# Optimization experiments

Measured on AMD Instinct MI355X. Metric: run time of the kernel, lower is better.

## Reference

```python
import jax, jax.numpy as jnp
import numpy as np

N_LOW, N_HIGH = 20000, 60000
E_LOW, E_L2H, E_HIGH = 320000, 540000, 480000
EPS = 1e-5
NEG_SLOPE = 0.2


def _gatv2(x_src, x_dst, edge_index, Wl, Wr, att, bias):
    """PyG GATv2Conv with concat heads, aggr='mean', no self loops.
    att: [H, C]. Returns [n_dst, H*C]."""
    H, C = att.shape
    n_dst = x_dst.shape[0]
    xl = (x_src @ Wl).reshape(-1, H, C)   # [n_src, H, C]
    xr = (x_dst @ Wr).reshape(-1, H, C)   # [n_dst, H, C]
    src, dst = edge_index[0], edge_index[1]
    z = jax.nn.leaky_relu(xl[src] + xr[dst], NEG_SLOPE)        # [E, H, C]
    logits = jnp.einsum('ehc,hc->eh', z, att)                  # [E, H]
    m = jax.ops.segment_max(logits, dst, num_segments=n_dst)   # segment softmax
    e = jnp.exp(logits - m[dst])
    s = jax.ops.segment_sum(e, dst, num_segments=n_dst)
    alpha = e / s[dst]                                         # [E, H]
    out = jax.ops.segment_sum(xl[src] * alpha[:, :, None], dst, num_segments=n_dst)
    deg = jax.ops.segment_sum(jnp.ones((src.shape[0],), out.dtype), dst, num_segments=n_dst)
    out = out / jnp.maximum(deg, 1.0)[:, None, None]           # aggr='mean'
    out = out.reshape(n_dst, H * C)
    if bias is not None:
        out = out + bias
    return out


def _bn(x, g, b):
    mu = x.mean(axis=0)
    var = x.var(axis=0)
    return (x - mu) * jax.lax.rsqrt(var + EPS) * g + b


def _forward(x_low, x_high, z_std, e_low, e_l2h, e_high,
             l1_Wl, l1_Wr, l1_att, l1_b, bn1_g, bn1_b,
             l2_Wl, l2_Wr, l2_att, l2_b, bn2_g, bn2_b,
             l3_Wl, l3_Wr, l3_att, l3_b,
             lh_Wl, lh_Wr, lh_att,
             h1_Wl, h1_Wr, h1_att, h1_b, bn3_g, bn3_b,
             h2_Wl, h2_Wr, h2_att, h2_b, bn4_g, bn4_b,
             h3_Wl, h3_Wr, h3_att, h3_b):
    # low_net: GATv2(125->128,h2) -> BN(256) -> GATv2(256->128) -> BN(128) -> GATv2(128->128)
    h = _gatv2(x_low, x_low, e_low, l1_Wl, l1_Wr, l1_att, l1_b)
    h = _bn(h, bn1_g, bn1_b)
    h = _gatv2(h, h, e_low, l2_Wl, l2_Wr, l2_att, l2_b)
    h = _bn(h, bn2_g, bn2_b)
    h = _gatv2(h, h, e_low, l3_Wl, l3_Wr, l3_att, l3_b)
    # bipartite low2high: (encod_low[128], x_high[1]) -> 128, no bias
    eh = _gatv2(h, x_high, e_l2h, lh_Wl, lh_Wr, lh_att, None)
    eh = jnp.concatenate([z_std, eh], axis=-1)                 # [N_HIGH, 129]
    # high_net
    g = _gatv2(eh, eh, e_high, h1_Wl, h1_Wr, h1_att, h1_b)
    g = _bn(g, bn3_g, bn3_b)
    g = _gatv2(g, g, e_high, h2_Wl, h2_Wr, h2_att, h2_b)
    g = _bn(g, bn4_g, bn4_b)
    return _gatv2(g, g, e_high, h3_Wl, h3_Wr, h3_att, h3_b)   # [N_HIGH, 2]


def setup_inputs() -> dict:
    key = jax.random.key(0)
    ks = iter(jax.random.split(key, 64))
    def P(shape, fan_in):
        return jax.random.normal(next(ks), shape, jnp.float32) / np.sqrt(fan_in)
    inp = {}
    inp['x_low'] = jax.random.normal(next(ks), (N_LOW, 125), jnp.float32)
    inp['x_high'] = jax.random.normal(next(ks), (N_HIGH, 1), jnp.float32)
    inp['z_std'] = jax.random.normal(next(ks), (N_HIGH, 1), jnp.float32)
    inp['e_low'] = jnp.stack([jax.random.randint(next(ks), (E_LOW,), 0, N_LOW),
                              jax.random.randint(next(ks), (E_LOW,), 0, N_LOW)])
    inp['e_l2h'] = jnp.stack([jax.random.randint(next(ks), (E_L2H,), 0, N_LOW),
                              jax.random.randint(next(ks), (E_L2H,), 0, N_HIGH)])
    inp['e_high'] = jnp.stack([jax.random.randint(next(ks), (E_HIGH,), 0, N_HIGH),
                               jax.random.randint(next(ks), (E_HIGH,), 0, N_HIGH)])
    inp['l1_Wl'] = P((125, 256), 125); inp['l1_Wr'] = P((125, 256), 125)
    inp['l1_att'] = P((2, 128), 128);  inp['l1_b'] = jnp.zeros((256,), jnp.float32)
    inp['bn1_g'] = jnp.ones((256,), jnp.float32); inp['bn1_b'] = jnp.zeros((256,), jnp.float32)
    inp['l2_Wl'] = P((256, 128), 256); inp['l2_Wr'] = P((256, 128), 256)
    inp['l2_att'] = P((1, 128), 128);  inp['l2_b'] = jnp.zeros((128,), jnp.float32)
    inp['bn2_g'] = jnp.ones((128,), jnp.float32); inp['bn2_b'] = jnp.zeros((128,), jnp.float32)
    inp['l3_Wl'] = P((128, 128), 128); inp['l3_Wr'] = P((128, 128), 128)
    inp['l3_att'] = P((1, 128), 128);  inp['l3_b'] = jnp.zeros((128,), jnp.float32)
    inp['lh_Wl'] = P((128, 128), 128); inp['lh_Wr'] = P((1, 128), 1)
    inp['lh_att'] = P((1, 128), 128)
    inp['h1_Wl'] = P((129, 256), 129); inp['h1_Wr'] = P((129, 256), 129)
    inp['h1_att'] = P((2, 128), 128);  inp['h1_b'] = jnp.zeros((256,), jnp.float32)
    inp['bn3_g'] = jnp.ones((256,), jnp.float32); inp['bn3_b'] = jnp.zeros((256,), jnp.float32)
    inp['h2_Wl'] = P((256, 128), 256); inp['h2_Wr'] = P((256, 128), 256)
    inp['h2_att'] = P((1, 128), 128);  inp['h2_b'] = jnp.zeros((128,), jnp.float32)
    inp['bn4_g'] = jnp.ones((128,), jnp.float32); inp['bn4_b'] = jnp.zeros((128,), jnp.float32)
    inp['h3_Wl'] = P((128, 2), 128);   inp['h3_Wr'] = P((128, 2), 128)
    inp['h3_att'] = P((1, 2), 2);      inp['h3_b'] = jnp.zeros((2,), jnp.float32)
    return inp


def reference(x_low, x_high, z_std, e_low, e_l2h, e_high,
              l1_Wl, l1_Wr, l1_att, l1_b, bn1_g, bn1_b,
              l2_Wl, l2_Wr, l2_att, l2_b, bn2_g, bn2_b,
              l3_Wl, l3_Wr, l3_att, l3_b,
              lh_Wl, lh_Wr, lh_att,
              h1_Wl, h1_Wr, h1_att, h1_b, bn3_g, bn3_b,
              h2_Wl, h2_Wr, h2_att, h2_b, bn4_g, bn4_b,
              h3_Wl, h3_Wr, h3_att, h3_b):
    return _forward(x_low, x_high, z_std, e_low, e_l2h, e_high,
                    l1_Wl, l1_Wr, l1_att, l1_b, bn1_g, bn1_b,
                    l2_Wl, l2_Wr, l2_att, l2_b, bn2_g, bn2_b,
                    l3_Wl, l3_Wr, l3_att, l3_b,
                    lh_Wl, lh_Wr, lh_att,
                    h1_Wl, h1_Wr, h1_att, h1_b, bn3_g, bn3_b,
                    h2_Wl, h2_Wr, h2_att, h2_b, bn4_g, bn4_b,
                    h3_Wl, h3_Wr, h3_att, h3_b)
```

## Files before the change

kernel.cpp:

```cpp
#include <hip/hip_runtime.h>
#include <hip/hip_bf16.h>
#include <cstdint>
#include <cstddef>
#include <cmath>

#define NEG_SLOPE 0.2f

#define PB  1024
#define CSH 10
#define CBS 1024
#define NBCMAX 160
#define PBN 2048

using frag = __attribute__((ext_vector_type(8))) short;
using facc = __attribute__((ext_vector_type(4))) float;

__device__ __forceinline__ float bf_hi(unsigned u) {
    union { unsigned i; float f; } t; t.i = u & 0xffff0000u; return t.f;
}
__device__ __forceinline__ float bf_lo(unsigned u) {
    union { unsigned i; float f; } t; t.i = u << 16; return t.f;
}
__device__ __forceinline__ void unpack8(uint4 u, float* v) {
    v[0] = bf_lo(u.x); v[1] = bf_hi(u.x);
    v[2] = bf_lo(u.y); v[3] = bf_hi(u.y);
    v[4] = bf_lo(u.z); v[5] = bf_hi(u.z);
    v[6] = bf_lo(u.w); v[7] = bf_hi(u.w);
}

typedef const __attribute__((address_space(1))) void* gas_cptr;
typedef __attribute__((address_space(3))) void* las_ptr;
__device__ __forceinline__ void gload_lds16(const __hip_bfloat16* g, __hip_bfloat16* l) {
    __builtin_amdgcn_global_load_lds((gas_cptr)(const void*)g, (las_ptr)(void*)l, 16, 0, 0);
}

__global__ __launch_bounds__(256)
void msplitA(const int* __restrict__ s0, const int* __restrict__ d0, int E0,
             const int* __restrict__ s1, const int* __restrict__ d1, int E1,
             const int* __restrict__ s2, const int* __restrict__ d2, int E2,
             int nc0, int nc1, int nc2, int cap0, int cap1, int cap2,
             int* __restrict__ stage, int* __restrict__ cnt2) {
    __shared__ int hist[NBCMAX];
    __shared__ int rbase[NBCMAX];
    __shared__ int curs[NBCMAX];
    __shared__ int ord[1024];
    __shared__ int obkt[1024];
    const int NBC = nc0 + nc1 + nc2;
    const long Etot = (long)E0 + E1 + E2;
    int tid = threadIdx.x;
    int lane = tid & 63;
    long chunk = (Etot + PB - 1) / PB;
    long c0 = (long)blockIdx.x * chunk;
    long c1 = c0 + chunk; if (c1 > Etot) c1 = Etot;
    const long sec1 = (long)PB * nc0 * cap0;
    const long sec2 = sec1 + (long)PB * nc1 * cap1;
    for (int t = tid; t < NBC; t += 256) curs[t] = 0;
    __syncthreads();
    for (long r0 = c0; r0 < c1; r0 += 1024) {
        int n = (int)((c1 - r0 < 1024) ? (c1 - r0) : 1024);
        for (int t = tid; t < NBC; t += 256) hist[t] = 0;
        __syncthreads();
        int mye[4], myb[4], myr[4];
#pragma unroll
        for (int k = 0; k < 4; ++k) {
            int li = k * 256 + tid;
            myb[k] = -1;
            if (li < n) {
                long i = r0 + li;
                int src, dst, gb;
                if (i < E0) { src = s0[i]; dst = d0[i]; gb = dst >> CSH; }
                else if (i < (long)E0 + E1) { long j = i - E0; src = s1[j]; dst = d1[j]; gb = nc0 + (dst >> CSH); }
                else { long j = i - E0 - E1; src = s2[j]; dst = d2[j]; gb = nc0 + nc1 + (dst >> CSH); }
                mye[k] = (src << CSH) | (dst & (CBS - 1));
                myb[k] = gb;
                myr[k] = atomicAdd(&hist[gb], 1);
            }
        }
        __syncthreads();
        if (tid < 64) {
            int carry = 0;
            for (int base = 0; base < NBC; base += 64) {
                int g = base + lane;
                int v = (g < NBC) ? hist[g] : 0;
                int sum = v;
#pragma unroll
                for (int o = 1; o < 64; o <<= 1) {
                    int t = __shfl_up(sum, o, 64);
                    if (lane >= o) sum += t;
                }
                if (g < NBC) rbase[g] = carry + sum - v;
                carry += __shfl(sum, 63, 64);
            }
        }
        __syncthreads();
#pragma unroll
        for (int k = 0; k < 4; ++k)
            if (myb[k] >= 0) {
                int pos = rbase[myb[k]] + myr[k];
                ord[pos] = mye[k];
                obkt[pos] = myb[k];
            }
        __syncthreads();
        for (int pos = tid; pos < n; pos += 256) {
            int b = obkt[pos];
            int rank = pos - rbase[b] + curs[b];
            long addr; int cap;
            if (b < nc0)            { cap = cap0; addr = (long)(blockIdx.x * nc0 + b) * cap0; }
            else if (b < nc0 + nc1) { cap = cap1; addr = sec1 + (long)(blockIdx.x * nc1 + (b - nc0)) * cap1; }
            else                    { cap = cap2; addr = sec2 + (long)(blockIdx.x * nc2 + (b - nc0 - nc1)) * cap2; }
            if (rank < cap) stage[addr + rank] = ord[pos];
        }
        __syncthreads();
        for (int t = tid; t < NBC; t += 256) curs[t] += hist[t];
        __syncthreads();
    }
    for (int t = tid; t < NBC; t += 256) {
        int cap = (t < nc0) ? cap0 : (t < nc0 + nc1) ? cap1 : cap2;
        int c = curs[t]; if (c > cap) c = cap;
        cnt2[(long)blockIdx.x * NBC + t] = c;
    }
}

__global__ void scanC1(const int* __restrict__ cnt2, int* __restrict__ tot, int NBC) {
    __shared__ int red[256];
    int gb = blockIdx.x;
    int tid = threadIdx.x;
    int s = 0;
    for (int p = tid; p < PB; p += 256) s += cnt2[(long)p * NBC + gb];
    red[tid] = s;
    __syncthreads();
    for (int o = 128; o; o >>= 1) {
        if (tid < o) red[tid] += red[tid + o];
        __syncthreads();
    }
    if (tid == 0) tot[gb] = red[0];
}

__global__ void scanC2(const int* __restrict__ tot, int* __restrict__ cstart,
                       int NBC, int nc0, int nc1) {
    if (threadIdx.x == 0) {
        int c = 0;
        for (int gb = 0; gb < NBC; ++gb) {
            if (gb == nc0 || gb == nc0 + nc1) c = 0;
            cstart[gb] = c;
            c += tot[gb];
        }
    }
}

__global__ __launch_bounds__(1024)
void fineB(const int* __restrict__ cnt2, const int* __restrict__ cstart,
           const int* __restrict__ stage,
           int nc0, int nc1, int nc2, int cap0, int cap1, int cap2,
           int* __restrict__ off0, int* __restrict__ col0, int n0,
           int* __restrict__ off1, int* __restrict__ col1, int n1,
           int* __restrict__ off2, int* __restrict__ col2, int n2) {
    __shared__ int fragb[PB + 1];
    __shared__ int cnt[1024];
    __shared__ int wsum[17];
    const int NBC = nc0 + nc1 + nc2;
    int gb = blockIdx.x;
    int tid = threadIdx.x;
    int lane = tid & 63;
    int wv = tid >> 6;
    int cb, ncg, n; long base2, stride; int* off; int* col;
    const long sec1 = (long)PB * nc0 * cap0;
    const long sec2 = sec1 + (long)PB * nc1 * cap1;
    if (gb < nc0) {
        cb = gb; ncg = nc0; n = n0; off = off0; col = col0;
        base2 = (long)cb * cap0; stride = (long)nc0 * cap0;
    } else if (gb < nc0 + nc1) {
        cb = gb - nc0; ncg = nc1; n = n1; off = off1; col = col1;
        base2 = sec1 + (long)cb * cap1; stride = (long)nc1 * cap1;
    } else {
        cb = gb - nc0 - nc1; ncg = nc2; n = n2; off = off2; col = col2;
        base2 = sec2 + (long)cb * cap2; stride = (long)nc2 * cap2;
    }
    int dlo = cb << CSH;
    int colbase = cstart[gb];
    int v = cnt2[(long)tid * NBC + gb];
    int sum = v;
#pragma unroll
    for (int o = 1; o < 64; o <<= 1) {
        int t = __shfl_up(sum, o, 64);
        if (lane >= o) sum += t;
    }
    if (lane == 63) wsum[wv] = sum;
    __syncthreads();
    if (tid == 0) {
        int c = 0;
        for (int w = 0; w < 16; ++w) { int t = wsum[w]; wsum[w] = c; c += t; }
        wsum[16] = c;
    }
    __syncthreads();
    fragb[tid] = wsum[wv] + sum - v;
    if (tid == 0) fragb[PB] = wsum[16];
    __syncthreads();
    int sz = fragb[PB];
    cnt[tid] = 0;
    __syncthreads();
    for (int p = tid; p < sz; p += 1024) {
        int lo = 0, hi = PB;
        while (hi - lo > 1) { int mid = (lo + hi) >> 1; if (fragb[mid] <= p) lo = mid; else hi = mid; }
        int e = stage[base2 + (long)lo * stride + (p - fragb[lo])];
        atomicAdd(&cnt[e & (CBS - 1)], 1);
    }
    __syncthreads();
    int cv = cnt[tid];
    int csum = cv;
#pragma unroll
    for (int o = 1; o < 64; o <<= 1) {
        int t = __shfl_up(csum, o, 64);
        if (lane >= o) csum += t;
    }
    if (lane == 63) wsum[wv] = csum;
    __syncthreads();
    if (tid == 0) {
        int c = 0;
        for (int w = 0; w < 16; ++w) { int t = wsum[w]; wsum[w] = c; c += t; }
    }
    __syncthreads();
    int excl = wsum[wv] + csum - cv;
    int d = dlo + tid;
    if (d < n) off[d] = colbase + excl;
    if (cb == ncg - 1 && tid == 0) off[n] = colbase + sz;
    __syncthreads();
    cnt[tid] = colbase + excl;
    __syncthreads();
    for (int p = tid; p < sz; p += 1024) {
        int lo = 0, hi = PB;
        while (hi - lo > 1) { int mid = (lo + hi) >> 1; if (fragb[mid] <= p) lo = mid; else hi = mid; }
        int e = stage[base2 + (long)lo * stride + (p - fragb[lo])];
        int pos = atomicAdd(&cnt[e & (CBS - 1)], 1);
        col[pos] = e >> CSH;
    }
}

template<int KP, int KSTEP>
__global__ __launch_bounds__(256)
void gemm_t(const __hip_bfloat16* __restrict__ A,
            const __hip_bfloat16* __restrict__ Bt,
            __hip_bfloat16* __restrict__ C,
            const float* __restrict__ bias, int M, int N) {
    constexpr int CPR = KSTEP / 8;
    constexpr int ITER = CPR / 2;
    __shared__ __hip_bfloat16 As[128 * KSTEP];
    __shared__ __hip_bfloat16 Bs[128 * KSTEP];
    int tid = threadIdx.x;
    int lane = tid & 63;
    int wave = tid >> 6;
    int wm = wave >> 1, wn = wave & 1;
    int quad = lane >> 4, l16 = lane & 15;
    int m0 = blockIdx.y * 128;
    int n0 = blockIdx.x * 128;

    facc acc[4][4] = {};

    for (int k0 = 0; k0 < KP; k0 += KSTEP) {
        if (k0) __syncthreads();
#pragma unroll
        for (int p = 0; p < ITER; ++p) {
            int idx = p * 256 + tid;
            int row = idx / CPR;
            int c = idx - row * CPR;
            int gr = m0 + row; if (gr >= M) gr = M - 1;
            int lbase = (p * 256 + wave * 64) * 8;
            gload_lds16(A + (size_t)gr * KP + k0 + c * 8, As + lbase);
            gload_lds16(Bt + (size_t)(n0 + row) * KP + k0 + c * 8, Bs + lbase);
        }
        __syncthreads();
#pragma unroll
        for (int kk = 0; kk < KSTEP / 32; ++kk) {
            frag a[4], b[4];
#pragma unroll
            for (int i = 0; i < 4; ++i) {
                a[i] = *(const frag*)(As + (wm * 64 + i * 16 + l16) * KSTEP + kk * 32 + quad * 8);
                b[i] = *(const frag*)(Bs + (wn * 64 + i * 16 + l16) * KSTEP + kk * 32 + quad * 8);
            }
#pragma unroll
            for (int i = 0; i < 4; ++i)
#pragma unroll
                for (int j = 0; j < 4; ++j)
                    acc[i][j] = __builtin_amdgcn_mfma_f32_16x16x32_bf16(b[j], a[i], acc[i][j], 0, 0, 0);
        }
    }

    float4 bv[4];
#pragma unroll
    for (int j = 0; j < 4; ++j) {
        int n = n0 + wn * 64 + j * 16 + quad * 4;
        if (bias != nullptr) bv[j] = *(const float4*)(bias + n);
        else { bv[j].x = 0.f; bv[j].y = 0.f; bv[j].z = 0.f; bv[j].w = 0.f; }
    }
#pragma unroll
    for (int i = 0; i < 4; ++i) {
        int m = m0 + wm * 64 + i * 16 + l16;
        if (m >= M) continue;
#pragma unroll
        for (int j = 0; j < 4; ++j) {
            int n = n0 + wn * 64 + j * 16 + quad * 4;
            union { uint2 u; __hip_bfloat16 hh[4]; } pk;
            pk.hh[0] = __float2bfloat16(acc[i][j][0] + bv[j].x);
            pk.hh[1] = __float2bfloat16(acc[i][j][1] + bv[j].y);
            pk.hh[2] = __float2bfloat16(acc[i][j][2] + bv[j].z);
            pk.hh[3] = __float2bfloat16(acc[i][j][3] + bv[j].w);
            *(uint2*)(C + (size_t)m * N + n) = pk.u;
        }
    }
}

__global__ void gemm_n22_bn(const __hip_bfloat16* __restrict__ A,
                            const float* __restrict__ Wl, const float* __restrict__ Wr,
                            const float* __restrict__ s, const float* __restrict__ t,
                            float* __restrict__ YL, float* __restrict__ YR, int M, int K) {
    int i = blockIdx.x * blockDim.x + threadIdx.x;
    if (i >= M) return;
    float l0 = 0.f, l1 = 0.f, r0 = 0.f, r1 = 0.f;
    const unsigned* a = (const unsigned*)(A + (size_t)i * K);
    for (int k2 = 0; k2 < K / 2; ++k2) {
        unsigned u = a[k2];
        int k = k2 * 2;
        float v0 = fmaf(bf_lo(u), s[k], t[k]);
        float v1 = fmaf(bf_hi(u), s[k + 1], t[k + 1]);
        l0 = fmaf(v0, Wl[k * 2 + 0], l0);
        l1 = fmaf(v0, Wl[k * 2 + 1], l1);
        l0 = fmaf(v1, Wl[k * 2 + 2], l0);
        l1 = fmaf(v1, Wl[k * 2 + 3], l1);
        r0 = fmaf(v0, Wr[k * 2 + 0], r0);
        r1 = fmaf(v0, Wr[k * 2 + 1], r1);
        r0 = fmaf(v1, Wr[k * 2 + 2], r0);
        r1 = fmaf(v1, Wr[k * 2 + 3], r1);
    }
    YL[(size_t)i * 2 + 0] = l0;
    YL[(size_t)i * 2 + 1] = l1;
    YR[(size_t)i * 2 + 0] = r0;
    YR[(size_t)i * 2 + 1] = r1;
}

__global__ void prep_all(const float* __restrict__ l1Wl, const float* __restrict__ l1Wr,
                         const float* __restrict__ lhWl,
                         const float* __restrict__ h1Wl, const float* __restrict__ h1Wr,
                         const float* __restrict__ x_low, const float* __restrict__ x_high,
                         const float* __restrict__ lhWr, const float* __restrict__ z_std,
                         __hip_bfloat16* __restrict__ w_l1, __hip_bfloat16* __restrict__ w_lh,
                         __hip_bfloat16* __restrict__ w_h1,
                         __hip_bfloat16* __restrict__ XLOWB, __hip_bfloat16* __restrict__ XRo,
                         __hip_bfloat16* __restrict__ EHB,
                         int o1, int o2, int o3, int o4, int o5, int o6, int o7, int o8) {
    int i = blockIdx.x * blockDim.x + threadIdx.x;
    if (i < o1) {
        int r = i >> 7, c = i & 127;
        XLOWB[i] = __float2bfloat16((c < 125) ? x_low[(size_t)r * 125 + c] : 0.f);
    } else if (i < o2) {
        int j = i - o1; int r = j >> 7, c = j & 127;
        XRo[j] = __float2bfloat16(x_high[r] * lhWr[c]);
    } else if (i < o3) {
        int j = i - o2; int r = j >> 5, c = (j & 31) + 128;
        EHB[(size_t)r * 160 + c] = __float2bfloat16((c == 128) ? z_std[r] : 0.f);
    } else if (i < o4) {
        int j = i - o3; int n = j >> 7, k = j & 127;
        w_l1[j] = __float2bfloat16((k < 125) ? l1Wl[(size_t)k * 256 + n] : 0.f);
    } else if (i < o5) {
        int j = i - o4; int n = j >> 7, k = j & 127;
        w_l1[256 * 128 + j] = __float2bfloat16((k < 125) ? l1Wr[(size_t)k * 256 + n] : 0.f);
    } else if (i < o6) {
        int j = i - o5; int n = j >> 7, k = j & 127;
        w_lh[j] = __float2bfloat16(lhWl[(size_t)k * 128 + n]);
    } else if (i < o7) {
        int j = i - o6; int n = j / 160, k = j - n * 160;
        float v = 0.f;
        if (k < 128) v = h1Wl[(size_t)(k + 1) * 256 + n];
        else if (k == 128) v = h1Wl[n];
        w_h1[j] = __float2bfloat16(v);
    } else if (i < o8) {
        int j = i - o7; int n = j / 160, k = j - n * 160;
        float v = 0.f;
        if (k < 128) v = h1Wr[(size_t)(k + 1) * 256 + n];
        else if (k == 128) v = h1Wr[n];
        w_h1[256 * 160 + j] = __float2bfloat16(v);
    }
}

__global__ void wconv_bnfold2(const float* __restrict__ Wl, const float* __restrict__ Wr,
                              const float* __restrict__ scale, const float* __restrict__ shift,
                              __hip_bfloat16* __restrict__ Wt, float* __restrict__ bout,
                              int K, int N, int Kp) {
    __shared__ float red[256];
    const float* W = blockIdx.y ? Wr : Wl;
    __hip_bfloat16* wt = Wt + (size_t)blockIdx.y * N * Kp;
    float* bo = bout + blockIdx.y * N;
    int n = blockIdx.x;
    int tid = threadIdx.x;
    float acc = 0.f;
    for (int k = tid; k < Kp; k += 256) {
        float v = 0.f;
        if (k < K) {
            float w = W[(size_t)k * N + n];
            v = w * scale[k];
            acc = fmaf(w, shift[k], acc);
        }
        wt[(size_t)n * Kp + k] = __float2bfloat16(v);
    }
    red[tid] = acc;
    __syncthreads();
    for (int o = 128; o; o >>= 1) {
        if (tid < o) red[tid] += red[tid + o];
        __syncthreads();
    }
    if (tid == 0) bo[n] = red[0];
}

__global__ void gat_c128_p2(const __hip_bfloat16* __restrict__ xl, int xls,
                            const __hip_bfloat16* __restrict__ xr, int xrs,
                            const int* __restrict__ row_off, const int* __restrict__ col,
                            const float* __restrict__ att, const float* __restrict__ bias,
                            __hip_bfloat16* __restrict__ outb, int obstride,
                            int n_dst) {
    int pair = (blockIdx.x * blockDim.x + threadIdx.x) >> 6;
    int lane = threadIdx.x & 63;
    int d = pair * 2 + (lane >> 5);
    int g = (lane >> 4) & 1;
    int q = lane & 15;
    int cb = q * 8;
    bool dvalid = d < n_dst;
    int dd = dvalid ? d : (n_dst - 1);
    int beg = row_off[dd], end = row_off[dd + 1];
    int deg = dvalid ? (end - beg) : 0;
    int md = deg;
    md = max(md, __shfl_xor(md, 32, 64));

    float xrv[8], av[8];
    unpack8(*(const uint4*)(xr + (size_t)dd * xrs + cb), xrv);
    {
        float4 a0 = *(const float4*)(att + cb);
        float4 a1 = *(const float4*)(att + cb + 4);
        av[0] = a0.x; av[1] = a0.y; av[2] = a0.z; av[3] = a0.w;
        av[4] = a1.x; av[5] = a1.y; av[6] = a1.z; av[7] = a1.w;
    }

    float s = 0.f;
    float acc[8] = {0.f, 0.f, 0.f, 0.f, 0.f, 0.f, 0.f, 0.f};

    if (md > 0) {
        bool pv = (g) < deg;
        int i0 = pv ? col[beg + g] : 0;
        uint4 u = *(const uint4*)(xl + (size_t)i0 * xls + cb);
        int i1 = 0;
        if (2 < md) { bool p1 = (2 + g) < deg; i1 = p1 ? col[beg + 2 + g] : 0; }

        for (int e = 0; e < md; e += 2) {
            bool have_next = (e + 2) < md;
            uint4 un;
            if (have_next)
                un = *(const uint4*)(xl + (size_t)i1 * xls + cb);
            int i2 = 0;
            if (e + 4 < md) { bool p2 = (e + 4 + g) < deg; i2 = p2 ? col[beg + e + 4 + g] : 0; }
            bool nv = (e + 2 + g) < deg;

            float v[8];
            unpack8(u, v);
            float p = 0.f;
#pragma unroll
            for (int c = 0; c < 8; ++c) {
                float z = v[c] + xrv[c];
                z = fmaxf(z, NEG_SLOPE * z);
                p = fmaf(z, av[c], p);
            }
            p += __shfl_xor(p, 8, 64);
            p += __shfl_xor(p, 4, 64);
            p += __shfl_xor(p, 2, 64);
            p += __shfl_xor(p, 1, 64);
            if (!pv) p = -INFINITY;
            float w = __expf(fminf(p, 85.f));
            s += w;
#pragma unroll
            for (int c = 0; c < 8; ++c) acc[c] = fmaf(w, v[c], acc[c]);

            if (have_next) { u = un; pv = nv; }
            i1 = i2;
        }
    }

    s += __shfl_xor(s, 16, 64);
#pragma unroll
    for (int c = 0; c < 8; ++c) acc[c] += __shfl_xor(acc[c], 16, 64);

    float inv = (deg > 0) ? 1.f / (s * (float)deg) : 0.f;
    float o8[8];
#pragma unroll
    for (int c = 0; c < 8; ++c) o8[c] = acc[c] * inv;
    if (bias != nullptr) {
#pragma unroll
        for (int c = 0; c < 8; ++c) o8[c] += bias[cb + c];
    }
    if (g == 0 && dvalid) {
        union { uint4 u; __hip_bfloat16 hh[8]; } pk;
#pragma unroll
        for (int c = 0; c < 8; ++c) pk.hh[c] = __float2bfloat16(o8[c]);
        *(uint4*)(outb + (size_t)d * obstride + cb) = pk.u;
    }
}

__global__ void gat_c256h2(const __hip_bfloat16* __restrict__ xl, int xls,
                           const __hip_bfloat16* __restrict__ xr, int xrs,
                           const int* __restrict__ row_off, const int* __restrict__ col,
                           const float* __restrict__ att, const float* __restrict__ bias,
                           __hip_bfloat16* __restrict__ outb, int obstride,
                           int n_dst) {
    int dst = (blockIdx.x * blockDim.x + threadIdx.x) >> 6;
    int lane = threadIdx.x & 63;
    if (dst >= n_dst) return;
    int g = lane >> 5;
    int q = lane & 31;
    int cb = q * 8;
    int beg = row_off[dst], end = row_off[dst + 1];

    float xrv[8], av[8];
    unpack8(*(const uint4*)(xr + (size_t)dst * xrs + cb), xrv);
    {
        float4 a0 = *(const float4*)(att + cb);
        float4 a1 = *(const float4*)(att + cb + 4);
        av[0] = a0.x; av[1] = a0.y; av[2] = a0.z; av[3] = a0.w;
        av[4] = a1.x; av[5] = a1.y; av[6] = a1.z; av[7] = a1.w;
    }

    float s = 0.f;
    float acc[8] = {0.f, 0.f, 0.f, 0.f, 0.f, 0.f, 0.f, 0.f};

    if (beg < end) {
        int e0g = beg + g;
        bool pv = e0g < end;
        int i0 = col[pv ? e0g : beg];
        uint4 u = *(const uint4*)(xl + (size_t)i0 * xls + cb);
        int e1g = beg + 2 + g;
        int i1 = (beg + 2 < end) ? col[(e1g < end) ? e1g : beg] : 0;

        for (int e0 = beg; e0 < end; e0 += 2) {
            bool have_next = (e0 + 2) < end;
            uint4 un;
            if (have_next)
                un = *(const uint4*)(xl + (size_t)i1 * xls + cb);
            int e2g = e0 + 4 + g;
            int i2 = (e0 + 4 < end) ? col[(e2g < end) ? e2g : beg] : 0;
            bool nv = (e0 + 2 + g) < end;

            float v[8];
            unpack8(u, v);
            float p = 0.f;
#pragma unroll
            for (int c = 0; c < 8; ++c) {
                float z = v[c] + xrv[c];
                z = fmaxf(z, NEG_SLOPE * z);
                p = fmaf(z, av[c], p);
            }
            p += __shfl_xor(p, 8, 64);
            p += __shfl_xor(p, 4, 64);
            p += __shfl_xor(p, 2, 64);
            p += __shfl_xor(p, 1, 64);
            if (!pv) p = -INFINITY;
            float w = __expf(fminf(p, 85.f));
            s += w;
#pragma unroll
            for (int c = 0; c < 8; ++c) acc[c] = fmaf(w, v[c], acc[c]);

            if (have_next) { u = un; pv = nv; }
            i1 = i2;
        }
    }

    s += __shfl_xor(s, 32, 64);
#pragma unroll
    for (int c = 0; c < 8; ++c) acc[c] += __shfl_xor(acc[c], 32, 64);

    int deg = end - beg;
    float inv = (deg > 0) ? 1.f / (s * (float)deg) : 0.f;
    float o8[8];
#pragma unroll
    for (int c = 0; c < 8; ++c) o8[c] = acc[c] * inv;
    if (bias != nullptr) {
#pragma unroll
        for (int c = 0; c < 8; ++c) o8[c] += bias[cb + c];
    }
    if (g == 0) {
        union { uint4 u; __hip_bfloat16 hh[8]; } pk;
#pragma unroll
        for (int c = 0; c < 8; ++c) pk.hh[c] = __float2bfloat16(o8[c]);
        *(uint4*)(outb + (size_t)dst * obstride + cb) = pk.u;
    }
}

__global__ void gat_c2(const float* __restrict__ xl, const float* __restrict__ xr,
                       const int* __restrict__ row_off, const int* __restrict__ col,
                       const float* __restrict__ att, const float* __restrict__ bias,
                       float* __restrict__ out, int n_dst) {
    int dst = blockIdx.x * blockDim.x + threadIdx.x;
    if (dst >= n_dst) return;
    float x0 = xr[(size_t)dst * 2], x1 = xr[(size_t)dst * 2 + 1];
    float a0 = att[0], a1 = att[1];
    int beg = row_off[dst], end = row_off[dst + 1];
    float s = 0.f, acc0 = 0.f, acc1 = 0.f;
    for (int e = beg; e < end; ++e) {
        int src = col[e];
        float v0 = xl[(size_t)src * 2], v1 = xl[(size_t)src * 2 + 1];
        float z0 = v0 + x0; z0 = fmaxf(z0, NEG_SLOPE * z0);
        float z1 = v1 + x1; z1 = fmaxf(z1, NEG_SLOPE * z1);
        float p = fmaf(z0, a0, z1 * a1);
        float w = __expf(fminf(p, 85.f));
        s += w;
        acc0 = fmaf(w, v0, acc0);
        acc1 = fmaf(w, v1, acc1);
    }
    int deg = end - beg;
    float o0 = 0.f, o1 = 0.f;
    if (deg > 0) {
        float inv = 1.f / (s * (float)deg);
        o0 = acc0 * inv;
        o1 = acc1 * inv;
    }
    out[(size_t)dst * 2 + 0] = o0 + bias[0];
    out[(size_t)dst * 2 + 1] = o1 + bias[1];
}

__global__ void bn_partial_d(const __hip_bfloat16* __restrict__ x, float* __restrict__ part,
                             int Nr, int rpb) {
    int C = blockDim.x;
    int c = threadIdx.x;
    int b = blockIdx.x;
    int r0 = b * rpb;
    int r1 = r0 + rpb; if (r1 > Nr) r1 = Nr;
    float s = 0.f, q = 0.f;
    for (int r = r0; r < r1; ++r) {
        float v = __bfloat162float(x[(size_t)r * C + c]);
        s += v;
        q = fmaf(v, v, q);
    }
    part[(size_t)b * C + c] = s;
    part[(size_t)PBN * 256 + (size_t)b * C + c] = q;
}

__global__ void bn_finalize_w(const float* __restrict__ part,
                              const float* __restrict__ g, const float* __restrict__ b,
                              float* __restrict__ scale, float* __restrict__ shift,
                              int Nr, int C) {
    int c = (blockIdx.x * blockDim.x + threadIdx.x) >> 6;
    int lane = threadIdx.x & 63;
    if (c >= C) return;
    float s = 0.f, q = 0.f;
    for (int blk = lane; blk < PBN; blk += 64) {
        s += part[(size_t)blk * C + c];
        q += part[(size_t)PBN * 256 + (size_t)blk * C + c];
    }
#pragma unroll
    for (int o = 32; o; o >>= 1) {
        s += __shfl_xor(s, o, 64);
        q += __shfl_xor(q, o, 64);
    }
    if (lane == 0) {
        float mu = s / (float)Nr;
        float var = q / (float)Nr - mu * mu;
        float inv = rsqrtf(var + 1e-5f);
        float a = g[c] * inv;
        scale[c] = a;
        shift[c] = b[c] - mu * a;
    }
}

extern "C" void kernel_launch(void* const* d_in, const int* in_sizes, int n_in,
                              void* d_out, int out_size, void* d_ws, size_t ws_size,
                              hipStream_t stream) {
    const float* x_low  = (const float*)d_in[0];
    const float* x_high = (const float*)d_in[1];
    const float* z_std  = (const float*)d_in[2];
    const int* e_low  = (const int*)d_in[3];
    const int* e_l2h  = (const int*)d_in[4];
    const int* e_high = (const int*)d_in[5];
    const float* l1_Wl = (const float*)d_in[6];
    const float* l1_Wr = (const float*)d_in[7];
    const float* l1_att = (const float*)d_in[8];
    const float* l1_b  = (const float*)d_in[9];
    const float* bn1_g = (const float*)d_in[10];
    const float* bn1_b = (const float*)d_in[11];
    const float* l2_Wl = (const float*)d_in[12];
    const float* l2_Wr = (const float*)d_in[13];
    const float* l2_att = (const float*)d_in[14];
    const float* l2_b  = (const float*)d_in[15];
    const float* bn2_g = (const float*)d_in[16];
    const float* bn2_b = (const float*)d_in[17];
    const float* l3_Wl = (const float*)d_in[18];
    const float* l3_Wr = (const float*)d_in[19];
    const float* l3_att = (const float*)d_in[20];
    const float* l3_b  = (const float*)d_in[21];
    const float* lh_Wl = (const float*)d_in[22];
    const float* lh_Wr = (const float*)d_in[23];
    const float* lh_att = (const float*)d_in[24];
    const float* h1_Wl = (const float*)d_in[25];
    const float* h1_Wr = (const float*)d_in[26];
    const float* h1_att = (const float*)d_in[27];
    const float* h1_b  = (const float*)d_in[28];
    const float* bn3_g = (const float*)d_in[29];
    const float* bn3_b = (const float*)d_in[30];
    const float* h2_Wl = (const float*)d_in[31];
    const float* h2_Wr = (const float*)d_in[32];
    const float* h2_att = (const float*)d_in[33];
    const float* h2_b  = (const float*)d_in[34];
    const float* bn4_g = (const float*)d_in[35];
    const float* bn4_b = (const float*)d_in[36];
    const float* h3_Wl = (const float*)d_in[37];
    const float* h3_Wr = (const float*)d_in[38];
    const float* h3_att = (const float*)d_in[39];
    const float* h3_b  = (const float*)d_in[40];

    const int N_low = in_sizes[0] / 125;
    const int N_high = in_sizes[1];
    const int E_low = in_sizes[3] / 2;
    const int E_l2h = in_sizes[4] / 2;
    const int E_high = in_sizes[5] / 2;

    char* ws = (char*)d_ws;
    size_t woff = 0;
    auto walloc = [&](size_t bytes) -> void* {
        void* p = (void*)(ws + woff);
        woff += (bytes + 255) & ~(size_t)255;
        return p;
    };
    __hip_bfloat16* XLR = (__hip_bfloat16*)walloc((size_t)N_high * 512 * 2);
    __hip_bfloat16* A1  = (__hip_bfloat16*)walloc((size_t)N_high * 256 * 2);
    __hip_bfloat16* A2  = (__hip_bfloat16*)walloc((size_t)N_high * 128 * 2);
    __hip_bfloat16* XRo = (__hip_bfloat16*)walloc((size_t)N_high * 128 * 2);
    __hip_bfloat16* XLOWB = (__hip_bfloat16*)walloc((size_t)N_low * 128 * 2);
    __hip_bfloat16* EHB = (__hip_bfloat16*)walloc((size_t)N_high * 160 * 2);
    float* YL = (float*)walloc((size_t)N_high * 2 * 4);
    float* YR = (float*)walloc((size_t)N_high * 2 * 4);
    int* off_low  = (int*)walloc((size_t)(N_low + 1) * 4);
    int* col_low  = (int*)walloc((size_t)E_low * 4);
    int* off_l2h  = (int*)walloc((size_t)(N_high + 1) * 4);
    int* col_l2h  = (int*)walloc((size_t)E_l2h * 4);
    int* off_high = (int*)walloc((size_t)(N_high + 1) * 4);
    int* col_high = (int*)walloc((size_t)E_high * 4);
    const int nc0 = (N_low + CBS - 1) >> CSH;
    const int nc1 = (N_high + CBS - 1) >> CSH;
    const int nc2 = (N_high + CBS - 1) >> CSH;
    const int NBC = nc0 + nc1 + nc2;
    const long Etot = (long)E_low + E_l2h + E_high;
    const long chunk = (Etot + PB - 1) / PB;
    auto capf = [&](int ng) {
        double m = (double)chunk * CBS / ng;
        int c = (int)(m + 8.0 * sqrt(m) + 16.0);
        return (c + 15) & ~15;
    };
    const int cap0 = capf(N_low);
    const int cap1 = capf(N_high);
    const int cap2 = capf(N_high);
    int* cnt2   = (int*)walloc((size_t)PB * NBC * 4);
    int* cstart = (int*)walloc((size_t)(NBC + 1) * 4);
    int* ctot   = (int*)walloc((size_t)(NBC + 1) * 4);
    float* bnpart = (float*)walloc((size_t)2 * PBN * 256 * 4);
    float* bnsc   = (float*)walloc(512 * 4);
    float* bb     = (float*)walloc(512 * 4);
    __hip_bfloat16* w_l1 = (__hip_bfloat16*)walloc(512 * 128 * 2);
    __hip_bfloat16* w_l2 = (__hip_bfloat16*)walloc(256 * 256 * 2);
    __hip_bfloat16* w_l3 = (__hip_bfloat16*)walloc(256 * 128 * 2);
    __hip_bfloat16* w_lh = (__hip_bfloat16*)walloc(128 * 128 * 2);
    __hip_bfloat16* w_h1 = (__hip_bfloat16*)walloc(512 * 160 * 2);
    __hip_bfloat16* w_h2 = (__hip_bfloat16*)walloc(256 * 256 * 2);

    int* stage = (int*)XLR;

    {
        int o1 = N_low * 128;
        int o2 = o1 + N_high * 128;
        int o3 = o2 + N_high * 32;
        int o4 = o3 + 256 * 128;
        int o5 = o4 + 256 * 128;
        int o6 = o5 + 128 * 128;
        int o7 = o6 + 256 * 160;
        int o8 = o7 + 256 * 160;
        prep_all<<<(o8 + 255) / 256, 256, 0, stream>>>(
            l1_Wl, l1_Wr, lh_Wl, h1_Wl, h1_Wr, x_low, x_high, lh_Wr, z_std,
            w_l1, w_lh, w_h1, XLOWB, XRo, EHB,
            o1, o2, o3, o4, o5, o6, o7, o8);
    }

    msplitA<<<PB, 256, 0, stream>>>(
        e_low, e_low + E_low, E_low,
        e_l2h, e_l2h + E_l2h, E_l2h,
        e_high, e_high + E_high, E_high,
        nc0, nc1, nc2, cap0, cap1, cap2, stage, cnt2);
    scanC1<<<NBC, 256, 0, stream>>>(cnt2, ctot, NBC);
    scanC2<<<1, 64, 0, stream>>>(ctot, cstart, NBC, nc0, nc1);
    fineB<<<NBC, 1024, 0, stream>>>(cnt2, cstart, stage,
                                    nc0, nc1, nc2, cap0, cap1, cap2,
                                    off_low, col_low, N_low,
                                    off_l2h, col_l2h, N_high,
                                    off_high, col_high, N_high);

    auto gemm = [&](const __hip_bfloat16* A, const __hip_bfloat16* Bt, __hip_bfloat16* C,
                    int M, int N, int Kp, const float* bias) {
        dim3 g(N / 128, (M + 127) / 128);
        if (Kp == 128)      gemm_t<128, 128><<<g, 256, 0, stream>>>(A, Bt, C, bias, M, N);
        else if (Kp == 160) gemm_t<160, 160><<<g, 256, 0, stream>>>(A, Bt, C, bias, M, N);
        else                gemm_t<256, 128><<<g, 256, 0, stream>>>(A, Bt, C, bias, M, N);
    };
    auto gat1 = [&](const __hip_bfloat16* xl, int xls, const __hip_bfloat16* xr, int xrs,
                    const int* roff, const int* colv,
                    const float* att, const float* bias,
                    __hip_bfloat16* outb, int obs, int n_dst) {
        long waves = (n_dst + 1) / 2;
        long thr = waves * 64;
        gat_c128_p2<<<(unsigned)((thr + 255) / 256), 256, 0, stream>>>(
            xl, xls, xr, xrs, roff, colv, att, bias, outb, obs, n_dst);
    };
    auto gat2 = [&](const __hip_bfloat16* xl, int xls, const __hip_bfloat16* xr, int xrs,
                    const int* roff, const int* colv,
                    const float* att, const float* bias,
                    __hip_bfloat16* outb, int obs, int n_dst) {
        long thr = (long)n_dst * 64;
        gat_c256h2<<<(unsigned)((thr + 255) / 256), 256, 0, stream>>>(
            xl, xls, xr, xrs, roff, colv, att, bias, outb, obs, n_dst);
    };
    auto bn_stats = [&](__hip_bfloat16* x, const float* g, const float* b, int Nr, int C) {
        int rpb = (Nr + PBN - 1) / PBN;
        bn_partial_d<<<PBN, C, 0, stream>>>(x, bnpart, Nr, rpb);
        bn_finalize_w<<<(C * 64 + 255) / 256, 256, 0, stream>>>(bnpart, g, b, bnsc, bnsc + 256, Nr, C);
    };
    auto fold2 = [&](const float* Wl, const float* Wr, __hip_bfloat16* Wt,
                     int K, int Nn, int Kp) {
        dim3 g(Nn, 2);
        wconv_bnfold2<<<g, 256, 0, stream>>>(Wl, Wr, bnsc, bnsc + 256, Wt, bb, K, Nn, Kp);
    };

    gemm(XLOWB, w_l1, XLR, N_low, 512, 128, nullptr);
    gat2(XLR, 512, XLR + 256, 512, off_low, col_low, l1_att, l1_b, A1, 256, N_low);
    bn_stats(A1, bn1_g, bn1_b, N_low, 256);

    fold2(l2_Wl, l2_Wr, w_l2, 256, 128, 256);
    gemm(A1, w_l2, XLR, N_low, 256, 256, bb);
    gat1(XLR, 256, XLR + 128, 256, off_low, col_low, l2_att, l2_b, A2, 128, N_low);
    bn_stats(A2, bn2_g, bn2_b, N_low, 128);

    fold2(l3_Wl, l3_Wr, w_l3, 128, 128, 128);
    gemm(A2, w_l3, XLR, N_low, 256, 128, bb);
    gat1(XLR, 256, XLR + 128, 256, off_low, col_low, l3_att, l3_b, A1, 128, N_low);

    gemm(A1, w_lh, XLR, N_low, 128, 128, nullptr);
    gat1(XLR, 128, XRo, 128, off_l2h, col_l2h, lh_att, nullptr, EHB, 160, N_high);

    gemm(EHB, w_h1, XLR, N_high, 512, 160, nullptr);
    gat2(XLR, 512, XLR + 256, 512, off_high, col_high, h1_att, h1_b, A1, 256, N_high);
    bn_stats(A1, bn3_g, bn3_b, N_high, 256);

    fold2(h2_Wl, h2_Wr, w_h2, 256, 128, 256);
    gemm(A1, w_h2, XLR, N_high, 256, 256, bb);
    gat1(XLR, 256, XLR + 128, 256, off_high, col_high, h2_att, h2_b, A2, 128, N_high);
    bn_stats(A2, bn4_g, bn4_b, N_high, 128);

    gemm_n22_bn<<<(N_high + 255) / 256, 256, 0, stream>>>(A2, h3_Wl, h3_Wr,
                                                          bnsc, bnsc + 256, YL, YR, N_high, 128);
    gat_c2<<<(N_high + 255) / 256, 256, 0, stream>>>(YL, YR, off_high, col_high,
                                                     h3_att, h3_b, (float*)d_out, N_high);
}
```

Baseline: 602.6 us.

## Sort CSR neighbor lists per row and swizzle GEMM block order

After the CSR build, each destination row's column list is sorted with an insertion sort, one thread per row. Sorted lists make the later gather of source rows in the GAT kernels more cache-friendly and also deterministic. The GEMM launch becomes a 1D grid that groups blocks in strips of 8 M-tiles so tiles sharing B columns run close together, padding the M tile count to a multiple of 8 and exiting early for out-of-range tiles. The sort adds serial per-thread work in fineB, which grows with row degree.

```diff
diff --git a/kernel.cpp b/kernel.cpp
--- a/kernel.cpp
+++ b/kernel.cpp
@@ -234,6 +234,17 @@
         int pos = atomicAdd(&cnt[e & (CBS - 1)], 1);
         col[pos] = e >> CSH;
     }
+    __syncthreads();
+    if (d < n) {
+        int b2 = colbase + excl;
+        int e2 = cnt[tid];
+        for (int i = b2 + 1; i < e2; ++i) {
+            int key = col[i];
+            int j = i - 1;
+            while (j >= b2 && col[j] > key) { col[j + 1] = col[j]; --j; }
+            col[j + 1] = key;
+        }
+    }
 }
 
 template<int KP, int KSTEP>
@@ -251,8 +262,14 @@
     int wave = tid >> 6;
     int wm = wave >> 1, wn = wave & 1;
     int quad = lane >> 4, l16 = lane & 15;
-    int m0 = blockIdx.y * 128;
-    int n0 = blockIdx.x * 128;
+
+    int NBx = N >> 7;
+    int lid = blockIdx.x;
+    int y = (lid & 7) + 8 * (lid / (8 * NBx));
+    int x = (lid >> 3) % NBx;
+    int m0 = y * 128;
+    if (m0 >= M) return;
+    int n0 = x * 128;
 
     facc acc[4][4] = {};
 
@@ -796,10 +813,13 @@
 
     auto gemm = [&](const __hip_bfloat16* A, const __hip_bfloat16* Bt, __hip_bfloat16* C,
                     int M, int N, int Kp, const float* bias) {
-        dim3 g(N / 128, (M + 127) / 128);
-        if (Kp == 128)      gemm_t<128, 128><<<g, 256, 0, stream>>>(A, Bt, C, bias, M, N);
-        else if (Kp == 160) gemm_t<160, 160><<<g, 256, 0, stream>>>(A, Bt, C, bias, M, N);
-        else                gemm_t<256, 128><<<g, 256, 0, stream>>>(A, Bt, C, bias, M, N);
+        int NBx = N / 128;
+        int My  = (M + 127) / 128;
+        int Myp = (My + 7) & ~7;
+        unsigned blocks = (unsigned)(NBx * Myp);
+        if (Kp == 128)      gemm_t<128, 128><<<blocks, 256, 0, stream>>>(A, Bt, C, bias, M, N);
+        else if (Kp == 160) gemm_t<160, 160><<<blocks, 256, 0, stream>>>(A, Bt, C, bias, M, N);
+        else                gemm_t<256, 128><<<blocks, 256, 0, stream>>>(A, Bt, C, bias, M, N);
     };
     auto gat1 = [&](const __hip_bfloat16* xl, int xls, const __hip_bfloat16* xr, int xrs,
                     const int* roff, const int* colv,
```

After: 699.8 us. 1.16x slower.
